# Optimization experiments

Hardware: AMD Instinct MI355X
Metric: run time of the kernel (lower is better)

## Reference

```python
import jax, jax.numpy as jnp
import numpy as np
from jax import lax

N, C_IN, L = 32, 256, 4096
C_OUT, K, GROUPS = 256, 9, 4
C_DIM, PAD, STRIDE = 128, 4, 1


def setup_inputs() -> dict:
    key = jax.random.key(0)
    k1, k2, k3, k4, k5 = jax.random.split(key, 5)
    x = jax.random.normal(k1, (N, C_IN, L), dtype=jnp.float32)
    c = jax.random.normal(k2, (N, C_DIM), dtype=jnp.float32)
    weight = jax.random.normal(k3, (C_OUT, C_IN // GROUPS, K), dtype=jnp.float32)
    c_weight = jax.random.normal(k4, (C_OUT, C_DIM), dtype=jnp.float32)
    bias = jax.random.normal(k5, (C_OUT,), dtype=jnp.float32)
    return {"x": x, "c": c, "weight": weight, "c_weight": c_weight, "bias": bias}


def reference(x, c, weight, c_weight, bias):
    # Grouped conv1d: equivalent to the unfold+per-group matmul in the torch code.
    # dims: x (N, C_in, L), weight (C_out, C_in/groups, K) -> out (N, C_out, L_out)
    out = lax.conv_general_dilated(
        x, weight,
        window_strides=(STRIDE,),
        padding=[(PAD, PAD)],
        dimension_numbers=("NCH", "OIH", "NCH"),
        feature_group_count=GROUPS,
    )
    # Concat-path context: cat([patches, c]) @ cat([W, cW]).T == conv(x) + c @ cW.T,
    # with the context term broadcast over all temporal positions.
    ctx = jnp.einsum("nd,od->no", c, c_weight)  # (N, C_out)
    out = out + ctx[:, :, None] + bias[None, :, None]
    return out
```

## Files before the change

kernel.cpp:

```cpp
#include <hip/hip_runtime.h>
#include <hip/hip_bf16.h>

#define NB     32
#define CIN    256
#define LIN    4096
#define COUT   256
#define KW     9
#define NGRP   4
#define CDIM   128
#define CPG    64
#define LT     256
#define LROWS  264
#define RSTR   72
#define WF_ELEMS (4*4*9*2*64*8)

typedef __attribute__((ext_vector_type(8))) short short8;
typedef __attribute__((ext_vector_type(4))) float float4v;

__global__ void pack_weights(const float* __restrict__ w, __hip_bfloat16* __restrict__ wF) {
    int tid = blockIdx.x * blockDim.x + threadIdx.x;
    if (tid >= WF_ELEMS) return;
    int j    = tid & 7;
    int lane = (tid >> 3) & 63;
    int rest = tid >> 9;
    int chunk = rest & 1;  rest >>= 1;
    int k     = rest % 9;  rest /= 9;
    int co16  = rest & 3;
    int g     = rest >> 2;
    int co = g * CPG + co16 * 16 + (lane & 15);
    int ci = chunk * 32 + (lane >> 4) * 8 + j;
    wF[tid] = __float2bfloat16(w[(co * CPG + ci) * KW + k]);
}

__global__ void ctx_kernel(const float* __restrict__ c, const float* __restrict__ cw,
                           const float* __restrict__ bias, float* __restrict__ ctxb) {
    int tid = blockIdx.x * blockDim.x + threadIdx.x;
    int n  = tid >> 8;
    int co = tid & 255;
    const float* cp = c  + n  * CDIM;
    const float* wp = cw + co * CDIM;
    float s = bias[co];
    #pragma unroll 4
    for (int d = 0; d < CDIM; ++d) s += cp[d] * wp[d];
    ctxb[tid] = s;
}

__global__ __launch_bounds__(256) void conv_mfma(
    const float* __restrict__ x, const __hip_bfloat16* __restrict__ wF,
    const float* __restrict__ ctxb, float* __restrict__ out)
{
    __shared__ __hip_bfloat16 xT[LROWS * RSTR];
    __shared__ float sctx[CPG];

    const int bx = blockIdx.x;
    const int t  = bx & 15;
    const int g  = (bx >> 4) & 3;
    const int n  = bx >> 6;
    const int l0 = t * LT;
    const int tid = threadIdx.x;

    if (tid < CPG) sctx[tid] = ctxb[n * COUT + g * CPG + tid];

    const float* xb = x + ((long)(n * CIN + g * CPG)) * LIN;
    for (int it = 0; it < 17; ++it) {
        int idx = it * 256 + tid;
        if (idx < 66 * 64) {
            int ci = idx & 63;
            int l4 = idx >> 6;
            int lg = l0 - 4 + 4 * l4;
            float4v v = {0.f, 0.f, 0.f, 0.f};
            if (lg >= 0 && lg < LIN)
                v = *(const float4v*)(xb + (long)ci * LIN + lg);
            int lb = 4 * l4;
            xT[(lb + 0) * RSTR + ci] = __float2bfloat16(v[0]);
            xT[(lb + 1) * RSTR + ci] = __float2bfloat16(v[1]);
            xT[(lb + 2) * RSTR + ci] = __float2bfloat16(v[2]);
            xT[(lb + 3) * RSTR + ci] = __float2bfloat16(v[3]);
        }
    }
    __syncthreads();

    const int lane = tid & 63;
    const int wv   = tid >> 6;
    const int r    = lane & 15;
    const int q    = lane >> 4;
    const int wl   = wv * 64;

    float4v acc[4][4];
    #pragma unroll
    for (int a = 0; a < 4; ++a)
        #pragma unroll
        for (int b = 0; b < 4; ++b)
            acc[a][b] = (float4v){0.f, 0.f, 0.f, 0.f};

    const short8* wFp = (const short8*)wF;

    #pragma unroll
    for (int k = 0; k < KW; ++k) {
        #pragma unroll
        for (int chunk = 0; chunk < 2; ++chunk) {
            short8 bfrag[4];
            #pragma unroll
            for (int l16 = 0; l16 < 4; ++l16) {
                int row = wl + l16 * 16 + r + k;
                bfrag[l16] = *(const short8*)(&xT[row * RSTR + chunk * 32 + q * 8]);
            }
            short8 afrag[4];
            #pragma unroll
            for (int co16 = 0; co16 < 4; ++co16) {
                afrag[co16] = wFp[(((g * 4 + co16) * 9 + k) * 2 + chunk) * 64 + lane];
            }
            #pragma unroll
            for (int co16 = 0; co16 < 4; ++co16)
                #pragma unroll
                for (int l16 = 0; l16 < 4; ++l16)
                    acc[co16][l16] = __builtin_amdgcn_mfma_f32_16x16x32_bf16(
                        afrag[co16], bfrag[l16], acc[co16][l16], 0, 0, 0);
        }
    }

    float* ob = out + ((long)(n * COUT + g * CPG)) * LIN + l0 + wl;
    #pragma unroll
    for (int co16 = 0; co16 < 4; ++co16) {
        #pragma unroll
        for (int reg = 0; reg < 4; ++reg) {
            int co_l = co16 * 16 + q * 4 + reg;
            float add = sctx[co_l];
            #pragma unroll
            for (int l16 = 0; l16 < 4; ++l16) {
                ob[(long)co_l * LIN + l16 * 16 + r] = acc[co16][l16][reg] + add;
            }
        }
    }
}

extern "C" void kernel_launch(void* const* d_in, const int* in_sizes, int n_in,
                              void* d_out, int out_size, void* d_ws, size_t ws_size,
                              hipStream_t stream) {
    const float* x   = (const float*)d_in[0];
    const float* c   = (const float*)d_in[1];
    const float* w   = (const float*)d_in[2];
    const float* cw  = (const float*)d_in[3];
    const float* bias= (const float*)d_in[4];
    float* out = (float*)d_out;

    __hip_bfloat16* wF = (__hip_bfloat16*)d_ws;
    float* ctxb = (float*)((char*)d_ws + (size_t)WF_ELEMS * 2);

    pack_weights<<<(WF_ELEMS + 255) / 256, 256, 0, stream>>>(w, wF);
    ctx_kernel<<<(NB * COUT) / 256, 256, 0, stream>>>(c, cw, bias, ctxb);
    conv_mfma<<<NB * NGRP * (LIN / LT), 256, 0, stream>>>(x, wF, ctxb, out);
}
```

Baseline: 273.7 us.

## Restructure x staging into LDS with packed bf16 stores and wave-per-output ctx reduction

```diff
diff --git a/kernel.cpp b/kernel.cpp
--- a/kernel.cpp
+++ b/kernel.cpp
@@ -10,12 +10,14 @@
 #define CDIM   128
 #define CPG    64
 #define LT     256
-#define LROWS  264
-#define RSTR   72
+#define NROWS  264
+#define RP     68
 #define WF_ELEMS (4*4*9*2*64*8)
 
 typedef __attribute__((ext_vector_type(8))) short short8;
+typedef __attribute__((ext_vector_type(4))) short short4v;
 typedef __attribute__((ext_vector_type(4))) float float4v;
+typedef __attribute__((ext_vector_type(4))) unsigned short ushort4v;
 
 __global__ void pack_weights(const float* __restrict__ w, __hip_bfloat16* __restrict__ wF) {
     int tid = blockIdx.x * blockDim.x + threadIdx.x;
@@ -32,24 +34,26 @@
     wF[tid] = __float2bfloat16(w[(co * CPG + ci) * KW + k]);
 }
 
-__global__ void ctx_kernel(const float* __restrict__ c, const float* __restrict__ cw,
-                           const float* __restrict__ bias, float* __restrict__ ctxb) {
-    int tid = blockIdx.x * blockDim.x + threadIdx.x;
-    int n  = tid >> 8;
-    int co = tid & 255;
-    const float* cp = c  + n  * CDIM;
-    const float* wp = cw + co * CDIM;
-    float s = bias[co];
-    #pragma unroll 4
-    for (int d = 0; d < CDIM; ++d) s += cp[d] * wp[d];
-    ctxb[tid] = s;
+__global__ __launch_bounds__(256) void ctx_kernel(const float* __restrict__ c,
+                                                  const float* __restrict__ cw,
+                                                  const float* __restrict__ bias,
+                                                  float* __restrict__ ctxb) {
+    int gw   = (blockIdx.x * 256 + threadIdx.x) >> 6;
+    int lane = threadIdx.x & 63;
+    int n  = gw >> 8;
+    int co = gw & 255;
+    float s = c[n * CDIM + lane]      * cw[co * CDIM + lane]
+            + c[n * CDIM + 64 + lane] * cw[co * CDIM + 64 + lane];
+    #pragma unroll
+    for (int off = 32; off; off >>= 1) s += __shfl_down(s, off);
+    if (lane == 0) ctxb[gw] = s + bias[co];
 }
 
-__global__ __launch_bounds__(256) void conv_mfma(
+__global__ __launch_bounds__(256, 4) void conv_mfma(
     const float* __restrict__ x, const __hip_bfloat16* __restrict__ wF,
     const float* __restrict__ ctxb, float* __restrict__ out)
 {
-    __shared__ __hip_bfloat16 xT[LROWS * RSTR];
+    __shared__ unsigned short sx[NROWS * RP];
     __shared__ float sctx[CPG];
 
     const int bx = blockIdx.x;
@@ -58,33 +62,60 @@
     const int n  = bx >> 6;
     const int l0 = t * LT;
     const int tid = threadIdx.x;
+    const int lane = tid & 63;
+    const int wv   = tid >> 6;
 
     if (tid < CPG) sctx[tid] = ctxb[n * COUT + g * CPG + tid];
 
-    const float* xb = x + ((long)(n * CIN + g * CPG)) * LIN;
-    for (int it = 0; it < 17; ++it) {
-        int idx = it * 256 + tid;
-        if (idx < 66 * 64) {
-            int ci = idx & 63;
-            int l4 = idx >> 6;
-            int lg = l0 - 4 + 4 * l4;
-            float4v v = {0.f, 0.f, 0.f, 0.f};
-            if (lg >= 0 && lg < LIN)
-                v = *(const float4v*)(xb + (long)ci * LIN + lg);
-            int lb = 4 * l4;
-            xT[(lb + 0) * RSTR + ci] = __float2bfloat16(v[0]);
-            xT[(lb + 1) * RSTR + ci] = __float2bfloat16(v[1]);
-            xT[(lb + 2) * RSTR + ci] = __float2bfloat16(v[2]);
-            xT[(lb + 3) * RSTR + ci] = __float2bfloat16(v[3]);
+    const float* xb = x + ((size_t)(n * CIN + g * CPG)) * LIN;
+
+    {
+        int q4  = 1 + (lane & 15);
+        int cqb = 4 * wv + (lane >> 4);
+        #pragma unroll
+        for (int i = 0; i < 4; ++i, q4 += 16) {
+            int lg = l0 - 4 + 4 * q4;
+            float4v v[4];
+            #pragma unroll
+            for (int j = 0; j < 4; ++j)
+                v[j] = *(const float4v*)(xb + (size_t)(4 * cqb + j) * LIN + lg);
+            int row = 4 * q4;
+            #pragma unroll
+            for (int d = 0; d < 4; ++d) {
+                ushort4v p;
+                #pragma unroll
+                for (int j = 0; j < 4; ++j)
+                    p[j] = __builtin_bit_cast(unsigned short, __float2bfloat16(v[j][d]));
+                *(ushort4v*)(&sx[(row + d) * RP + 4 * cqb]) = p;
+            }
+        }
+    }
+    if (tid < 32) {
+        int head = (tid < 16);
+        int q4 = head ? 0 : 65;
+        int cq = tid & 15;
+        int lg = l0 - 4 + 4 * q4;
+        bool ok = head ? (t > 0) : (t < 15);
+        float4v v[4];
+        #pragma unroll
+        for (int j = 0; j < 4; ++j)
+            v[j] = ok ? *(const float4v*)(xb + (size_t)(4 * cq + j) * LIN + lg)
+                      : (float4v){0.f, 0.f, 0.f, 0.f};
+        int row = 4 * q4;
+        #pragma unroll
+        for (int d = 0; d < 4; ++d) {
+            ushort4v p;
+            #pragma unroll
+            for (int j = 0; j < 4; ++j)
+                p[j] = __builtin_bit_cast(unsigned short, __float2bfloat16(v[j][d]));
+            *(ushort4v*)(&sx[(row + d) * RP + 4 * cq]) = p;
         }
     }
     __syncthreads();
 
-    const int lane = tid & 63;
-    const int wv   = tid >> 6;
-    const int r    = lane & 15;
-    const int q    = lane >> 4;
-    const int wl   = wv * 64;
+    const int r  = lane & 15;
+    const int q  = lane >> 4;
+    const int wl = wv * 64;
 
     float4v acc[4][4];
     #pragma unroll
@@ -103,7 +134,10 @@
             #pragma unroll
             for (int l16 = 0; l16 < 4; ++l16) {
                 int row = wl + l16 * 16 + r + k;
-                bfrag[l16] = *(const short8*)(&xT[row * RSTR + chunk * 32 + q * 8]);
+                int base = row * RP + chunk * 32 + q * 8;
+                short4v lo = *(const short4v*)(&sx[base]);
+                short4v hi = *(const short4v*)(&sx[base + 4]);
+                bfrag[l16] = __builtin_shufflevector(lo, hi, 0, 1, 2, 3, 4, 5, 6, 7);
             }
             short8 afrag[4];
             #pragma unroll
@@ -119,7 +153,7 @@
         }
     }
 
-    float* ob = out + ((long)(n * COUT + g * CPG)) * LIN + l0 + wl;
+    float* ob = out + ((size_t)(n * COUT + g * CPG)) * LIN + l0 + wl;
     #pragma unroll
     for (int co16 = 0; co16 < 4; ++co16) {
         #pragma unroll
@@ -128,7 +162,7 @@
             float add = sctx[co_l];
             #pragma unroll
             for (int l16 = 0; l16 < 4; ++l16) {
-                ob[(long)co_l * LIN + l16 * 16 + r] = acc[co16][l16][reg] + add;
+                ob[(size_t)co_l * LIN + l16 * 16 + r] = acc[co16][l16][reg] + add;
             }
         }
     }
@@ -137,17 +171,17 @@
 extern "C" void kernel_launch(void* const* d_in, const int* in_sizes, int n_in,
                               void* d_out, int out_size, void* d_ws, size_t ws_size,
                               hipStream_t stream) {
-    const float* x   = (const float*)d_in[0];
-    const float* c   = (const float*)d_in[1];
-    const float* w   = (const float*)d_in[2];
-    const float* cw  = (const float*)d_in[3];
-    const float* bias= (const float*)d_in[4];
+    const float* x    = (const float*)d_in[0];
+    const float* c    = (const float*)d_in[1];
+    const float* w    = (const float*)d_in[2];
+    const float* cw   = (const float*)d_in[3];
+    const float* bias = (const float*)d_in[4];
     float* out = (float*)d_out;
 
     __hip_bfloat16* wF = (__hip_bfloat16*)d_ws;
     float* ctxb = (float*)((char*)d_ws + (size_t)WF_ELEMS * 2);
 
     pack_weights<<<(WF_ELEMS + 255) / 256, 256, 0, stream>>>(w, wF);
-    ctx_kernel<<<(NB * COUT) / 256, 256, 0, stream>>>(c, cw, bias, ctxb);
+    ctx_kernel<<<(NB * COUT * 64) / 256, 256, 0, stream>>>(c, cw, bias, ctxb);
     conv_mfma<<<NB * NGRP * (LIN / LT), 256, 0, stream>>>(x, wF, ctxb, out);
 }
```

After: 259.9 us. 5.0% less time.
